# Kernel optimization log

Measured on AMD Instinct MI355X. Metric: run time of the kernel, lower is better.

Reference implementation:

```python
import jax, jax.numpy as jnp
import numpy as np

DIM = 128        # per-head dim == model width in this module
Q_HEADS = 16
KV_HEADS = 4
WINDOW = 512
BATCH = 4
SEQ = 2048


def setup_inputs() -> dict:
    key = jax.random.key(0)
    k1, k2, k3 = jax.random.split(key, 3)
    x = jax.random.normal(k1, (BATCH, SEQ, DIM), dtype=jnp.float32)
    # fused qkv weight, stored (in, out) so forward is x @ W_qkv
    W_qkv = jax.random.normal(k2, (DIM, (Q_HEADS + 2 * KV_HEADS) * DIM), dtype=jnp.float32) * (DIM ** -0.5)
    W_proj = jax.random.normal(k3, (Q_HEADS * DIM, DIM), dtype=jnp.float32) * ((Q_HEADS * DIM) ** -0.5)
    return {"x": x, "W_qkv": W_qkv, "W_proj": W_proj}


def _gqa_forward(x, W_qkv, W_proj):
    b, s, d = x.shape
    qkv = x @ W_qkv                                    # [b, s, (Hq+2Hkv)*d]
    qkv = qkv.reshape(b, s, Q_HEADS + 2 * KV_HEADS, d).transpose(0, 2, 1, 3)
    q = qkv[:, :Q_HEADS]                               # [b, Hq, s, d]
    k = qkv[:, Q_HEADS:Q_HEADS + KV_HEADS]             # [b, Hkv, s, d]
    v = qkv[:, Q_HEADS + KV_HEADS:]                    # [b, Hkv, s, d]

    # GQA: repeat kv heads to match q heads
    group = Q_HEADS // KV_HEADS
    k = jnp.repeat(k, group, axis=1)                   # [b, Hq, s, d]
    v = jnp.repeat(v, group, axis=1)

    scale = 1.0 / jnp.sqrt(jnp.float32(d))
    scores = jnp.einsum('bhqd,bhkd->bhqk', q, k) * scale   # [b, Hq, s, s]

    q_idx = jnp.arange(s)[:, None]
    kv_idx = jnp.arange(s)[None, :]
    rel = (q_idx - kv_idx).astype(jnp.float32)         # [s, s]
    # per-head ALiBi slope: exp2(-(h+1)*8/Hq), added (sign matches source)
    h = jnp.arange(Q_HEADS, dtype=jnp.float32)
    slopes = jnp.exp2(-((h + 1.0) * 8.0 / Q_HEADS))    # [Hq]
    scores = scores + slopes[None, :, None, None] * rel[None, None, :, :]

    mask = (q_idx >= kv_idx) & ((q_idx - kv_idx) <= WINDOW)
    scores = jnp.where(mask[None, None], scores, -jnp.inf)
    probs = jax.nn.softmax(scores, axis=-1)

    att = jnp.einsum('bhqk,bhkd->bhqd', probs, v)      # [b, Hq, s, d]
    att = att.transpose(0, 2, 1, 3).reshape(b, s, Q_HEADS * d)
    return att @ W_proj                                # [b, s, d]


def reference(x, W_qkv, W_proj):
    return _gqa_forward(x, W_qkv, W_proj)
```

## Files before the change

### kernel.cpp

```cpp
#include <hip/hip_runtime.h>
#include <math.h>

#define DIM_    128
#define QH_     16
#define KVH_    4
#define WIN_    512
#define BATCH_  4
#define SEQ_    2048
#define QKV_LD  3072

#define QB_LD   3136
#define VG_LD   2112
#define AH_LD   2112
#define WP_LD   2112

#define NX   (BATCH_*SEQ_*DIM_)
#define NWQ  (DIM_*QKV_LD)

typedef __attribute__((ext_vector_type(8))) short short8;
typedef __attribute__((ext_vector_type(4))) float f32x4;
typedef unsigned short u16;
typedef unsigned int u32;

__device__ __forceinline__ u16 f2bf(float f) {
    u32 u = __float_as_uint(f);
    u += 0x7fff + ((u >> 16) & 1);
    return (u16)(u >> 16);
}
__device__ __forceinline__ float bf2f(u16 u) {
    return __uint_as_float(((u32)u) << 16);
}
__device__ __forceinline__ u32 pkbf(float a, float b) {
    u32 r;
    __asm__("v_cvt_pk_bf16_f32 %0, %1, %2" : "=v"(r) : "v"(a), "v"(b));
    return r;
}
#define MFMA16 __builtin_amdgcn_mfma_f32_16x16x32_bf16

#if __has_builtin(__builtin_amdgcn_exp2f)
#define EXP2F __builtin_amdgcn_exp2f
#else
#define EXP2F exp2f
#endif

__device__ __forceinline__ void gload_lds16(const u16* g, u16* l) {
    __builtin_amdgcn_global_load_lds(
        (const __attribute__((address_space(1))) unsigned int*)(const void*)g,
        (__attribute__((address_space(3))) unsigned int*)(void*)l, 16, 0, 0);
}

__global__ __launch_bounds__(256) void prep(
    const float* __restrict__ x, const float* __restrict__ Wqkv,
    const float* __restrict__ Wproj,
    u16* __restrict__ xh, u16* __restrict__ wth, u16* __restrict__ wpth)
{
    if (blockIdx.x < 1024) {
        const size_t t = (size_t)blockIdx.x * 256 + threadIdx.x;
        float4 v = *(const float4*)(x + 4 * t);
        ushort4 o;
        o.x = f2bf(v.x); o.y = f2bf(v.y); o.z = f2bf(v.z); o.w = f2bf(v.w);
        *(ushort4*)(xh + 4 * t) = o;
        return;
    }
    __shared__ float T[32][33];
    int tile = blockIdx.x - 1024;
    const float* src; u16* dst; int N, ldo;
    if (tile < 384) { src = Wqkv;  dst = wth;  N = 3072; ldo = 128; }
    else { tile -= 384; src = Wproj; dst = wpth; N = 128; ldo = WP_LD; }
    const int ntile = N >> 5;
    const int k0 = (tile / ntile) << 5, n0 = (tile % ntile) << 5;
    const int tx = threadIdx.x & 31, ty = threadIdx.x >> 5;
    #pragma unroll
    for (int i = 0; i < 4; ++i)
        T[ty + 8 * i][tx] = src[(size_t)(k0 + ty + 8 * i) * N + n0 + tx];
    __syncthreads();
    #pragma unroll
    for (int i = 0; i < 4; ++i)
        dst[(size_t)(n0 + ty + 8 * i) * ldo + k0 + tx] = f2bf(T[tx][ty + 8 * i]);
}

__global__ __launch_bounds__(256) void gemm1_mfma(
    const u16* __restrict__ xh, const u16* __restrict__ wth,
    u16* __restrict__ qkvb, u16* __restrict__ vg)
{
    const int bn = blockIdx.x * 256;
    const int mc = blockIdx.y * 128;
    const int tid = threadIdx.x;
    const int wv = tid >> 6, lane = tid & 63;
    const int lo = lane & 15, hi = lane >> 4;
    const int lr = lo, quad = hi;
    const int wn = bn + wv * 64;

    __shared__ u16 Ct[2][16][264];

    short8 bf[4][4];
    #pragma unroll
    for (int nt = 0; nt < 4; ++nt)
        #pragma unroll
        for (int s = 0; s < 4; ++s)
            bf[nt][s] = *(const short8*)(
                wth + (size_t)(wn + nt * 16 + lo) * DIM_ + s * 32 + hi * 8);

    const bool qk = (bn < 2560);
    const u16* aA = xh + (size_t)(mc + lo) * DIM_ + hi * 8;
    const int sr = tid >> 4, sc = tid & 15;

#define G1BODY(AF, IT) do {                                                   \
    f32x4 acc[4] = {};                                                        \
    if (qk) {                                                                 \
        _Pragma("unroll")                                                     \
        for (int s = 0; s < 4; ++s)                                           \
            _Pragma("unroll")                                                 \
            for (int nt = 0; nt < 4; ++nt)                                    \
                acc[nt] = MFMA16(bf[nt][s], AF[s], acc[nt], 0, 0, 0);         \
        const int bufq = (IT) & 1;                                            \
        _Pragma("unroll")                                                     \
        for (int nt = 0; nt < 4; ++nt) {                                      \
            uint2 o;                                                          \
            o.x = pkbf(acc[nt][0], acc[nt][1]);                               \
            o.y = pkbf(acc[nt][2], acc[nt][3]);                               \
            *(uint2*)&Ct[bufq][lr][wv * 64 + nt * 16 + quad * 4] = o;         \
        }                                                                     \
        __syncthreads();                                                      \
        const int row = mc + (IT) * 16 + sr;                                  \
        u16* drow = qkvb + (size_t)row * QB_LD + bn;                          \
        short8 v0 = *(const short8*)&Ct[bufq][sr][sc * 8];                    \
        short8 v1 = *(const short8*)&Ct[bufq][sr][128 + sc * 8];              \
        *(short8*)(drow + sc * 8) = v0;                                       \
        *(short8*)(drow + 128 + sc * 8) = v1;                                 \
    } else {                                                                  \
        _Pragma("unroll")                                                     \
        for (int s = 0; s < 4; ++s)                                           \
            _Pragma("unroll")                                                 \
            for (int nt = 0; nt < 4; ++nt)                                    \
                acc[nt] = MFMA16(AF[s], bf[nt][s], acc[nt], 0, 0, 0);         \
        const int m0 = mc + (IT) * 16 + quad * 4;                             \
        const int bb = m0 >> 11, mseq = m0 & 2047;                            \
        _Pragma("unroll")                                                     \
        for (int nt = 0; nt < 4; ++nt) {                                      \
            const int ncol = wn + nt * 16 + lr - 2560;                        \
            const int kvh = ncol >> 7, d = ncol & 127;                        \
            uint2 o;                                                          \
            o.x = pkbf(acc[nt][0], acc[nt][1]);                               \
            o.y = pkbf(acc[nt][2], acc[nt][3]);                               \
            *(uint2*)(vg + ((size_t)(bb * KVH_ + kvh) * DIM_ + d) * VG_LD     \
                      + mseq) = o;                                            \
        }                                                                     \
    }                                                                         \
} while (0)

    short8 afA[4], afB[4];
    #pragma unroll
    for (int s = 0; s < 4; ++s) afA[s] = *(const short8*)(aA + s * 32);

    #pragma unroll 1
    for (int it = 0; it < 8; it += 2) {
        const u16* aN = aA + (size_t)(it + 1) * 16 * DIM_;
        #pragma unroll
        for (int s = 0; s < 4; ++s) afB[s] = *(const short8*)(aN + s * 32);
        G1BODY(afA, it);
        const int nx = (it + 2 < 8) ? (it + 2) : 7;
        const u16* aN2 = aA + (size_t)nx * 16 * DIM_;
        #pragma unroll
        for (int s = 0; s < 4; ++s) afA[s] = *(const short8*)(aN2 + s * 32);
        G1BODY(afB, it + 1);
    }
#undef G1BODY
}

__global__ __launch_bounds__(512) void attn_mfma(
    const u16* __restrict__ qkvb, const u16* __restrict__ vg,
    u16* __restrict__ ah)
{
    const int xcd  = blockIdx.x & 7;
    const int idx  = blockIdx.x >> 3;
    const int pair = xcd + 8 * (idx & 1);
    const int qt   = idx >> 1;
    const int b    = pair >> 2, kvh = pair & 3;
    const int q0 = qt << 5;
    const int tid = threadIdx.x;
    const int wv8 = tid >> 6, lane = tid & 63;
    const int hq = wv8 >> 1, mrow = wv8 & 1;
    const int lr = lane & 15, quad = lane >> 4;
    const int h = kvh * 4 + hq;
    const bool oddq = (quad & 1) != 0;

    __shared__ u16 Kb[2][16][512];
    __shared__ u16 Vb[2][16][512];

    const float scale2 = 0.08838834764831845f * 1.4426950408889634f;
    const float slope2 = exp2f(-0.5f * (float)(h + 1)) * 1.4426950408889634f;
    const int jbase = max(0, q0 - WIN_);
    const int nch = (q0 + 32 - jbase + 63) >> 6;
    const size_t rowb = (size_t)b * SEQ_;
    const u16* kgp = qkvb + rowb * QB_LD + (QH_ + kvh) * DIM_;
    const u16* vgb = vg + (size_t)(b * KVH_ + kvh) * DIM_ * VG_LD;
    const int lo = lane & 15, hi = lane >> 4;

    short8 qf[4];
    {
        const u16* qp = qkvb + (rowb + q0 + mrow * 16 + lr) * QB_LD
                        + h * DIM_ + quad * 8;
        #pragma unroll
        for (int s = 0; s < 4; ++s) qf[s] = *(const short8*)(qp + 32 * s);
    }

    float alpha0;
    {
        const int q = q0 + mrow * 16 + lr;
        const int rm = (q < WIN_) ? q : WIN_;
        alpha0 = slope2 * (float)(q - rm);
    }

    f32x4 O[8] = {};
    float rs = 0.f;

    #define STAGE(CH, SLOT) do {                                              \
        const int _jk = jbase + ((CH) << 6);                                  \
        _Pragma("unroll")                                                     \
        for (int _t = 0; _t < 2; ++_t) {                                      \
            const int _p = wv8 + _t * 8;                                      \
            int _kr = _jk + (_p >> 2) * 16 + lo;                              \
            _kr = (_kr < SEQ_) ? _kr : (SEQ_ - 1);                            \
            gload_lds16(kgp + (size_t)_kr * QB_LD + (_p & 3) * 32 + hi * 8,   \
                        &Kb[(SLOT)][_p][0]);                                  \
            int _kc = _jk + (_p & 1) * 32 + hi * 8;                           \
            _kc = (_kc < SEQ_ - 8) ? _kc : (SEQ_ - 8);                        \
            gload_lds16(vgb + (size_t)((_p >> 1) * 16 + lo) * VG_LD + _kc,    \
                        &Vb[(SLOT)][_p][0]);                                  \
        }                                                                     \
    } while (0)

    STAGE(0, 0);

    for (int ch = 0; ch < nch; ++ch) {
        const int jk = jbase + (ch << 6);
        const int slot = ch & 1;
        __asm__ volatile("s_waitcnt vmcnt(0)" ::: "memory");
        __asm__ volatile("s_barrier" ::: "memory");
        if (ch + 1 < nch) STAGE(ch + 1, slot ^ 1);

        u32 pw[4][2];
        const int qm0 = q0 + mrow * 16;
        #pragma unroll
        for (int nt = 0; nt < 4; ++nt) {
            f32x4 c = {0.f, 0.f, 0.f, 0.f};
            __builtin_amdgcn_s_setprio(1);
            #pragma unroll
            for (int s = 0; s < 4; ++s) {
                short8 kf = *(const short8*)&Kb[slot][nt * 4 + s][lane * 8];
                c = MFMA16(kf, qf[s], c, 0, 0, 0);
            }
            __builtin_amdgcn_s_setprio(0);
            const int jknt = jk + nt * 16;
            const float b0 = fmaf(-slope2, (float)(jknt + quad * 4), alpha0);
            float e0, e1, e2, e3;
            if (qm0 >= jknt + 15 && qm0 + 15 <= jknt + WIN_) {
                e0 = EXP2F(fmaf(c[0], scale2, b0));
                e1 = EXP2F(fmaf(c[1], scale2, b0 - slope2));
                e2 = EXP2F(fmaf(c[2], scale2, b0 - 2.f * slope2));
                e3 = EXP2F(fmaf(c[3], scale2, b0 - 3.f * slope2));
            } else {
                const int q = qm0 + lr, j0q = jknt + quad * 4;
                float ee[4];
                #pragma unroll
                for (int r = 0; r < 4; ++r) {
                    const int rel = q - (j0q + r);
                    const float t = fmaf(c[r], scale2, b0 - (float)r * slope2);
                    ee[r] = ((unsigned)rel <= (unsigned)WIN_) ? EXP2F(t) : 0.f;
                }
                e0 = ee[0]; e1 = ee[1]; e2 = ee[2]; e3 = ee[3];
            }
            rs += (e0 + e1) + (e2 + e3);
            pw[nt][0] = pkbf(e0, e1);
            pw[nt][1] = pkbf(e2, e3);
        }

        short8 pa[2];
        #pragma unroll
        for (int g = 0; g < 2; ++g) {
            union { u32 w[4]; short8 s; } P;
            #pragma unroll
            for (int w = 0; w < 2; ++w) {
                auto r = __builtin_amdgcn_permlane32_swap(
                    pw[2 * g][w], pw[2 * g + 1][w], false, false);
                const u32 rx = r[0], ry = r[1];
                const u32 sx = (u32)__shfl_xor((int)rx, 16);
                const u32 sy = (u32)__shfl_xor((int)ry, 16);
                P.w[w]     = oddq ? sy : rx;
                P.w[2 + w] = oddq ? ry : sx;
            }
            pa[g] = P.s;
        }

        __builtin_amdgcn_s_setprio(1);
        #pragma unroll
        for (int nt = 0; nt < 8; ++nt) {
            short8 vf0 = *(const short8*)&Vb[slot][nt * 2][lane * 8];
            short8 vf1 = *(const short8*)&Vb[slot][nt * 2 + 1][lane * 8];
            O[nt] = MFMA16(vf0, pa[0], O[nt], 0, 0, 0);
            O[nt] = MFMA16(vf1, pa[1], O[nt], 0, 0, 0);
        }
        __builtin_amdgcn_s_setprio(0);
    }
    #undef STAGE

    __asm__ volatile("s_waitcnt vmcnt(0)" ::: "memory");

    rs += __shfl_xor(rs, 16);
    rs += __shfl_xor(rs, 32);

    {
        const float inv = 1.0f / rs;
        u16* dst = ah + (rowb + q0 + mrow * 16 + lr) * (size_t)AH_LD
                   + h * DIM_;
        #pragma unroll
        for (int nt = 0; nt < 8; ++nt) {
            uint2 o;
            o.x = pkbf(O[nt][0] * inv, O[nt][1] * inv);
            o.y = pkbf(O[nt][2] * inv, O[nt][3] * inv);
            *(uint2*)(dst + nt * 16 + quad * 4) = o;
        }
    }
}

__global__ __launch_bounds__(512) void gemm2_mfma(
    const u16* __restrict__ ah, const u16* __restrict__ wpth,
    float* __restrict__ out)
{
    const int bm = blockIdx.x * 16;
    const int tid = threadIdx.x;
    const int wv8 = tid >> 6, lane = tid & 63;
    const int wc = wv8;
    const int lr = lane & 15, quad = lane >> 4;

    __shared__ u16 At2[2][16][520];

    #define G2STAGE(KS, SLOT) do {                                            \
        _Pragma("unroll")                                                     \
        for (int _t = 0; _t < 2; ++_t) {                                      \
            const int _r = wv8 * 2 + _t;                                      \
            gload_lds16(ah + (size_t)(bm + _r) * AH_LD + (KS) * 512           \
                        + lane * 8, &At2[(SLOT)][_r][0]);                     \
        }                                                                     \
    } while (0)

    f32x4 acc = {0.f, 0.f, 0.f, 0.f};

    G2STAGE(0, 0);

    #pragma unroll 1
    for (int ks = 0; ks < 4; ++ks) {
        const int slot = ks & 1;
        __asm__ volatile("s_waitcnt vmcnt(0)" ::: "memory");
        __asm__ volatile("s_barrier" ::: "memory");
        if (ks < 3) G2STAGE(ks + 1, slot ^ 1);

        const u16* wbase = wpth + (size_t)(wc * 16 + lr) * WP_LD
                           + ks * 512 + quad * 8;
        #pragma unroll
        for (int s = 0; s < 16; ++s) {
            short8 wf = *(const short8*)(wbase + s * 32);
            short8 af = *(const short8*)&At2[slot][lr][s * 32 + quad * 8];
            acc = MFMA16(wf, af, acc, 0, 0, 0);
        }
    }
    #undef G2STAGE

    __asm__ volatile("s_waitcnt vmcnt(0)" ::: "memory");

    {
        float* orow = out + (size_t)(bm + lr) * DIM_ + wc * 16 + quad * 4;
        *(float4*)orow = *(float4*)&acc;
    }
}

extern "C" void kernel_launch(void* const* d_in, const int* in_sizes, int n_in,
                              void* d_out, int out_size, void* d_ws, size_t ws_size,
                              hipStream_t stream)
{
    const float* x     = (const float*)d_in[0];
    const float* Wqkv  = (const float*)d_in[1];
    const float* Wproj = (const float*)d_in[2];
    float* out = (float*)d_out;

    u16* xh   = (u16*)d_ws;
    u16* wth  = xh   + (size_t)NX;
    u16* wpth = wth  + (size_t)NWQ;
    u16* qkvb = wpth + (size_t)DIM_ * WP_LD;
    u16* vg   = qkvb + (size_t)8192 * QB_LD;
    u16* ahp  = vg   + (size_t)BATCH_ * KVH_ * DIM_ * VG_LD;

    prep<<<1024 + 640, 256, 0, stream>>>(x, Wqkv, Wproj, xh, wth, wpth);

    gemm1_mfma<<<dim3(12, 64), 256, 0, stream>>>(xh, wth, qkvb, vg);

    attn_mfma<<<1024, 512, 0, stream>>>(qkvb, vg, ahp);

    gemm2_mfma<<<8192 / 16, 512, 0, stream>>>(ahp, wpth, out);
}
```

Before: 178.7 us.

## Process two query heads per wave in attention, halving block size

Each wave now computes two GQA query heads that share the same KV head instead of one. The attention block shrinks from 8 to 4 waves, and each wave issues twice the staging loads. The aim is to reuse each K/V fragment read from LDS across two MFMAs, cutting LDS traffic and per-head overhead. The cost is higher register pressure from doubled accumulators and Q fragments, which may lower occupancy, and fewer waves per block to hide the softmax latency.

New measurement: 190.2 us. 6.4% more time.

```diff
diff --git a/kernel.cpp b/kernel.cpp
--- a/kernel.cpp
+++ b/kernel.cpp
@@ -168,7 +168,7 @@
 #undef G1BODY
 }
 
-__global__ __launch_bounds__(512) void attn_mfma(
+__global__ __launch_bounds__(256) void attn_mfma(
     const u16* __restrict__ qkvb, const u16* __restrict__ vg,
     u16* __restrict__ ah)
 {
@@ -179,17 +179,24 @@
     const int b    = pair >> 2, kvh = pair & 3;
     const int q0 = qt << 5;
     const int tid = threadIdx.x;
-    const int wv8 = tid >> 6, lane = tid & 63;
-    const int hq = wv8 >> 1, mrow = wv8 & 1;
+    const int wv4 = tid >> 6, lane = tid & 63;
+    const int hp = wv4 >> 1, mrow = wv4 & 1;
     const int lr = lane & 15, quad = lane >> 4;
-    const int h = kvh * 4 + hq;
     const bool oddq = (quad & 1) != 0;
 
     __shared__ u16 Kb[2][16][512];
     __shared__ u16 Vb[2][16][512];
 
     const float scale2 = 0.08838834764831845f * 1.4426950408889634f;
-    const float slope2 = exp2f(-0.5f * (float)(h + 1)) * 1.4426950408889634f;
+    float slope2[2], alpha0[2];
+    #pragma unroll
+    for (int u = 0; u < 2; ++u) {
+        const int hu = kvh * 4 + hp * 2 + u;
+        slope2[u] = exp2f(-0.5f * (float)(hu + 1)) * 1.4426950408889634f;
+        const int q = q0 + mrow * 16 + lr;
+        const int rm = (q < WIN_) ? q : WIN_;
+        alpha0[u] = slope2[u] * (float)(q - rm);
+    }
     const int jbase = max(0, q0 - WIN_);
     const int nch = (q0 + 32 - jbase + 63) >> 6;
     const size_t rowb = (size_t)b * SEQ_;
@@ -197,29 +204,24 @@
     const u16* vgb = vg + (size_t)(b * KVH_ + kvh) * DIM_ * VG_LD;
     const int lo = lane & 15, hi = lane >> 4;
 
-    short8 qf[4];
-    {
+    short8 qf[2][4];
+    #pragma unroll
+    for (int u = 0; u < 2; ++u) {
+        const int hu = kvh * 4 + hp * 2 + u;
         const u16* qp = qkvb + (rowb + q0 + mrow * 16 + lr) * QB_LD
-                        + h * DIM_ + quad * 8;
-        #pragma unroll
-        for (int s = 0; s < 4; ++s) qf[s] = *(const short8*)(qp + 32 * s);
-    }
-
-    float alpha0;
-    {
-        const int q = q0 + mrow * 16 + lr;
-        const int rm = (q < WIN_) ? q : WIN_;
-        alpha0 = slope2 * (float)(q - rm);
-    }
-
-    f32x4 O[8] = {};
-    float rs = 0.f;
+                        + hu * DIM_ + quad * 8;
+        #pragma unroll
+        for (int s = 0; s < 4; ++s) qf[u][s] = *(const short8*)(qp + 32 * s);
+    }
+
+    f32x4 O[2][8] = {};
+    float rs[2] = {0.f, 0.f};
 
     #define STAGE(CH, SLOT) do {                                              \
         const int _jk = jbase + ((CH) << 6);                                  \
         _Pragma("unroll")                                                     \
-        for (int _t = 0; _t < 2; ++_t) {                                      \
-            const int _p = wv8 + _t * 8;                                      \
+        for (int _t = 0; _t < 4; ++_t) {                                      \
+            const int _p = wv4 + _t * 4;                                      \
             int _kr = _jk + (_p >> 2) * 16 + lo;                              \
             _kr = (_kr < SEQ_) ? _kr : (SEQ_ - 1);                            \
             gload_lds16(kgp + (size_t)_kr * QB_LD + (_p & 3) * 32 + hi * 8,   \
@@ -240,66 +242,78 @@
         __asm__ volatile("s_barrier" ::: "memory");
         if (ch + 1 < nch) STAGE(ch + 1, slot ^ 1);
 
-        u32 pw[4][2];
+        u32 pw[2][4][2];
         const int qm0 = q0 + mrow * 16;
         #pragma unroll
         for (int nt = 0; nt < 4; ++nt) {
-            f32x4 c = {0.f, 0.f, 0.f, 0.f};
+            f32x4 c0 = {0.f, 0.f, 0.f, 0.f}, c1 = {0.f, 0.f, 0.f, 0.f};
             __builtin_amdgcn_s_setprio(1);
             #pragma unroll
             for (int s = 0; s < 4; ++s) {
                 short8 kf = *(const short8*)&Kb[slot][nt * 4 + s][lane * 8];
-                c = MFMA16(kf, qf[s], c, 0, 0, 0);
+                c0 = MFMA16(kf, qf[0][s], c0, 0, 0, 0);
+                c1 = MFMA16(kf, qf[1][s], c1, 0, 0, 0);
             }
             __builtin_amdgcn_s_setprio(0);
             const int jknt = jk + nt * 16;
-            const float b0 = fmaf(-slope2, (float)(jknt + quad * 4), alpha0);
-            float e0, e1, e2, e3;
-            if (qm0 >= jknt + 15 && qm0 + 15 <= jknt + WIN_) {
-                e0 = EXP2F(fmaf(c[0], scale2, b0));
-                e1 = EXP2F(fmaf(c[1], scale2, b0 - slope2));
-                e2 = EXP2F(fmaf(c[2], scale2, b0 - 2.f * slope2));
-                e3 = EXP2F(fmaf(c[3], scale2, b0 - 3.f * slope2));
-            } else {
-                const int q = qm0 + lr, j0q = jknt + quad * 4;
-                float ee[4];
+            #pragma unroll
+            for (int u = 0; u < 2; ++u) {
+                const f32x4 c = u ? c1 : c0;
+                const float b0 = fmaf(-slope2[u], (float)(jknt + quad * 4),
+                                      alpha0[u]);
+                float e0, e1, e2, e3;
+                if (qm0 >= jknt + 15 && qm0 + 15 <= jknt + WIN_) {
+                    e0 = EXP2F(fmaf(c[0], scale2, b0));
+                    e1 = EXP2F(fmaf(c[1], scale2, b0 - slope2[u]));
+                    e2 = EXP2F(fmaf(c[2], scale2, b0 - 2.f * slope2[u]));
+                    e3 = EXP2F(fmaf(c[3], scale2, b0 - 3.f * slope2[u]));
+                } else {
+                    const int q = qm0 + lr, j0q = jknt + quad * 4;
+                    float ee[4];
+                    #pragma unroll
+                    for (int r = 0; r < 4; ++r) {
+                        const int rel = q - (j0q + r);
+                        const float t = fmaf(c[r], scale2,
+                                             b0 - (float)r * slope2[u]);
+                        ee[r] = ((unsigned)rel <= (unsigned)WIN_) ? EXP2F(t)
+                                                                  : 0.f;
+                    }
+                    e0 = ee[0]; e1 = ee[1]; e2 = ee[2]; e3 = ee[3];
+                }
+                rs[u] += (e0 + e1) + (e2 + e3);
+                pw[u][nt][0] = pkbf(e0, e1);
+                pw[u][nt][1] = pkbf(e2, e3);
+            }
+        }
+
+        short8 pa[2][2];
+        #pragma unroll
+        for (int u = 0; u < 2; ++u)
+            #pragma unroll
+            for (int g = 0; g < 2; ++g) {
+                union { u32 w[4]; short8 s; } P;
                 #pragma unroll
-                for (int r = 0; r < 4; ++r) {
-                    const int rel = q - (j0q + r);
-                    const float t = fmaf(c[r], scale2, b0 - (float)r * slope2);
-                    ee[r] = ((unsigned)rel <= (unsigned)WIN_) ? EXP2F(t) : 0.f;
+                for (int w = 0; w < 2; ++w) {
+                    auto r = __builtin_amdgcn_permlane32_swap(
+                        pw[u][2 * g][w], pw[u][2 * g + 1][w], false, false);
+                    const u32 rx = r[0], ry = r[1];
+                    const u32 sx = (u32)__shfl_xor((int)rx, 16);
+                    const u32 sy = (u32)__shfl_xor((int)ry, 16);
+                    P.w[w]     = oddq ? sy : rx;
+                    P.w[2 + w] = oddq ? ry : sx;
                 }
-                e0 = ee[0]; e1 = ee[1]; e2 = ee[2]; e3 = ee[3];
+                pa[u][g] = P.s;
             }
-            rs += (e0 + e1) + (e2 + e3);
-            pw[nt][0] = pkbf(e0, e1);
-            pw[nt][1] = pkbf(e2, e3);
-        }
-
-        short8 pa[2];
-        #pragma unroll
-        for (int g = 0; g < 2; ++g) {
-            union { u32 w[4]; short8 s; } P;
-            #pragma unroll
-            for (int w = 0; w < 2; ++w) {
-                auto r = __builtin_amdgcn_permlane32_swap(
-                    pw[2 * g][w], pw[2 * g + 1][w], false, false);
-                const u32 rx = r[0], ry = r[1];
-                const u32 sx = (u32)__shfl_xor((int)rx, 16);
-                const u32 sy = (u32)__shfl_xor((int)ry, 16);
-                P.w[w]     = oddq ? sy : rx;
-                P.w[2 + w] = oddq ? ry : sx;
-            }
-            pa[g] = P.s;
-        }
 
         __builtin_amdgcn_s_setprio(1);
         #pragma unroll
         for (int nt = 0; nt < 8; ++nt) {
             short8 vf0 = *(const short8*)&Vb[slot][nt * 2][lane * 8];
             short8 vf1 = *(const short8*)&Vb[slot][nt * 2 + 1][lane * 8];
-            O[nt] = MFMA16(vf0, pa[0], O[nt], 0, 0, 0);
-            O[nt] = MFMA16(vf1, pa[1], O[nt], 0, 0, 0);
+            O[0][nt] = MFMA16(vf0, pa[0][0], O[0][nt], 0, 0, 0);
+            O[1][nt] = MFMA16(vf0, pa[1][0], O[1][nt], 0, 0, 0);
+            O[0][nt] = MFMA16(vf1, pa[0][1], O[0][nt], 0, 0, 0);
+            O[1][nt] = MFMA16(vf1, pa[1][1], O[1][nt], 0, 0, 0);
         }
         __builtin_amdgcn_s_setprio(0);
     }
@@ -307,18 +321,23 @@
 
     __asm__ volatile("s_waitcnt vmcnt(0)" ::: "memory");
 
-    rs += __shfl_xor(rs, 16);
-    rs += __shfl_xor(rs, 32);
-
-    {
-        const float inv = 1.0f / rs;
+    #pragma unroll
+    for (int u = 0; u < 2; ++u) {
+        rs[u] += __shfl_xor(rs[u], 16);
+        rs[u] += __shfl_xor(rs[u], 32);
+    }
+
+    #pragma unroll
+    for (int u = 0; u < 2; ++u) {
+        const int hu = kvh * 4 + hp * 2 + u;
+        const float inv = 1.0f / rs[u];
         u16* dst = ah + (rowb + q0 + mrow * 16 + lr) * (size_t)AH_LD
-                   + h * DIM_;
+                   + hu * DIM_;
         #pragma unroll
         for (int nt = 0; nt < 8; ++nt) {
             uint2 o;
-            o.x = pkbf(O[nt][0] * inv, O[nt][1] * inv);
-            o.y = pkbf(O[nt][2] * inv, O[nt][3] * inv);
+            o.x = pkbf(O[u][nt][0] * inv, O[u][nt][1] * inv);
+            o.y = pkbf(O[u][nt][2] * inv, O[u][nt][3] * inv);
             *(uint2*)(dst + nt * 16 + quad * 4) = o;
         }
     }
@@ -395,7 +414,7 @@
 
     gemm1_mfma<<<dim3(12, 64), 256, 0, stream>>>(xh, wth, qkvb, vg);
 
-    attn_mfma<<<1024, 512, 0, stream>>>(qkvb, vg, ahp);
+    attn_mfma<<<1024, 256, 0, stream>>>(qkvb, vg, ahp);
 
     gemm2_mfma<<<8192 / 16, 512, 0, stream>>>(ahp, wpth, out);
 }
```
